# Optimization experiments

Measured on AMD Instinct MI355X. Metric: run time of the kernel, lower is better.

The kernel has to match this reference:

```python
import jax, jax.numpy as jnp
import numpy as np

NUM_CLASSES = 256


def setup_inputs() -> dict:
    key = jax.random.key(0)
    k1, k2 = jax.random.split(key)
    B = 524288
    logits = jax.random.normal(k1, (B, NUM_CLASSES), dtype=jnp.float32)
    targets = jax.random.randint(k2, (B,), 0, NUM_CLASSES, dtype=jnp.int64)
    return {"logits": logits, "targets": targets}


def reference(logits, targets):
    # cumulative logits along class dim: (B, C)
    cum = jnp.cumsum(logits, axis=1)
    C = logits.shape[1]
    # only thresholds k in [0, C-2] contribute (original loops range(C-1))
    ks = jnp.arange(C - 1)  # (C-1,)
    cum = cum[:, : C - 1]  # (B, C-1)
    # if k < target: loss += -logsigmoid(-cum[k]); else: loss += -logsigmoid(cum[k])
    sign = jnp.where(ks[None, :] < targets[:, None], -1.0, 1.0)  # (B, C-1)
    per_elem = -jax.nn.log_sigmoid(sign * cum)
    per_sample = jnp.sum(per_elem, axis=1)  # (B,)
    return jnp.mean(per_sample)
```

## Files before the change

kernel.cpp:

```cpp
#include <hip/hip_runtime.h>
#include <hip/hip_bf16.h>


#define WAVE 64
#define BLOCK 256
#define WPB (BLOCK / WAVE)
#define ROWS 8
#define NCLASS 256

__device__ __forceinline__ float wave_incl_scan(float s) {
    int t;
    t = __builtin_amdgcn_update_dpp(0, __float_as_int(s), 0x111, 0xf, 0xf, true); s += __int_as_float(t);
    t = __builtin_amdgcn_update_dpp(0, __float_as_int(s), 0x112, 0xf, 0xf, true); s += __int_as_float(t);
    t = __builtin_amdgcn_update_dpp(0, __float_as_int(s), 0x114, 0xf, 0xf, true); s += __int_as_float(t);
    t = __builtin_amdgcn_update_dpp(0, __float_as_int(s), 0x118, 0xf, 0xf, true); s += __int_as_float(t);
    t = __builtin_amdgcn_update_dpp(0, __float_as_int(s), 0x142, 0xa, 0xf, true); s += __int_as_float(t);
    t = __builtin_amdgcn_update_dpp(0, __float_as_int(s), 0x143, 0xc, 0xf, true); s += __int_as_float(t);
    return s;
}

template <bool EXACT>
__global__ __launch_bounds__(BLOCK) void ordloss_main(
        const float* __restrict__ logits,
        const int*   __restrict__ targets,
        double*      __restrict__ partials,
        int B) {
    const int lane = threadIdx.x & (WAVE - 1);
    const int wib  = threadIdx.x >> 6;
    const long long rowBase = ((long long)blockIdx.x * WPB + wib) * ROWS;
    const float lm = (lane == WAVE - 1) ? 0.0f : 1.0f;
    const int k0 = lane << 2;
    const float LOG2E = 1.4426950408889634f;

    const float4* p = reinterpret_cast<const float4*>(logits) + rowBase * (NCLASS / 4) + lane;

    float4 v[ROWS];
    int    tg[ROWS];
    #pragma unroll
    for (int i = 0; i < ROWS; ++i) {
        if (EXACT || rowBase + i < B) {
            v[i]  = p[i * (NCLASS / 4)];
            tg[i] = targets[rowBase + i];
        } else {
            v[i] = make_float4(0.f, 0.f, 0.f, 0.f);
            tg[i] = 0;
        }
    }

    float acc_lin = 0.0f, acc_abs = 0.0f, acc_log = 0.0f;
    #pragma unroll
    for (int i = 0; i < ROWS; ++i) {
        if (!EXACT && rowBase + i >= B) break;
        const int t = tg[i];

        const float l0 = v[i].x;
        const float l1 = l0 + v[i].y;
        const float l2 = l1 + v[i].z;
        const float l3 = l2 + v[i].w;

        const float incl = wave_incl_scan(l3);
        const float excl = incl - l3;

        const float c0 = excl + l0;
        const float c1 = excl + l1;
        const float c2 = excl + l2;
        const float c3 = excl + l3;

        const float a0 = fabsf(c0), a1 = fabsf(c1), a2 = fabsf(c2), a3 = fabsf(c3);

        const float u0 = __builtin_amdgcn_exp2f(-a0 * LOG2E);
        const float u1 = __builtin_amdgcn_exp2f(-a1 * LOG2E);
        const float u2 = __builtin_amdgcn_exp2f(-a2 * LOG2E);
        const float u3 = __builtin_amdgcn_exp2f(-a3 * LOG2E) * lm;

        float pr = 1.0f + u0;
        pr = __builtin_fmaf(pr, u1, pr);
        pr = __builtin_fmaf(pr, u2, pr);
        pr = __builtin_fmaf(pr, u3, pr);
        acc_log += __logf(pr);

        acc_abs += a0 + a1 + a2 + a3 * lm;

        const float sum_c = c0 + c1 + c2 + c3 * lm;
        float pre = 0.0f;
        pre += (k0 + 0 < t) ? c0 : 0.0f;
        pre += (k0 + 1 < t) ? c1 : 0.0f;
        pre += (k0 + 2 < t) ? c2 : 0.0f;
        pre += (k0 + 3 < t) ? c3 : 0.0f;
        acc_lin += 2.0f * pre - sum_c;
    }

    double d = 0.5 * ((double)acc_lin + (double)acc_abs) + (double)acc_log;
    #pragma unroll
    for (int off = 32; off > 0; off >>= 1)
        d += __shfl_down(d, off, WAVE);

    __shared__ double sd[WPB];
    if (lane == 0) sd[wib] = d;
    __syncthreads();
    if (threadIdx.x == 0) {
        double s = 0.0;
        #pragma unroll
        for (int w = 0; w < WPB; ++w) s += sd[w];
        partials[blockIdx.x] = s;
    }
}

__global__ __launch_bounds__(512) void ordloss_reduce(
        const double* __restrict__ partials, int n,
        float* __restrict__ out, double invB) {
    __shared__ double smem[512];
    double s = 0.0;
    for (int i = threadIdx.x; i < n; i += 512) s += partials[i];
    smem[threadIdx.x] = s;
    __syncthreads();
    for (int st = 256; st > 0; st >>= 1) {
        if (threadIdx.x < st) smem[threadIdx.x] += smem[threadIdx.x + st];
        __syncthreads();
    }
    if (threadIdx.x == 0) out[0] = (float)(smem[0] * invB);
}

extern "C" void kernel_launch(void* const* d_in, const int* in_sizes, int n_in,
                              void* d_out, int out_size, void* d_ws, size_t ws_size,
                              hipStream_t stream) {
    const float* logits   = (const float*)d_in[0];
    const int*   targets  = (const int*)d_in[1];
    float*       out      = (float*)d_out;
    double*      partials = (double*)d_ws;

    const int B = in_sizes[1];
    const int rows_per_block = WPB * ROWS;
    const int NB = (B + rows_per_block - 1) / rows_per_block;

    if (B % rows_per_block == 0)
        ordloss_main<true><<<NB, BLOCK, 0, stream>>>(logits, targets, partials, B);
    else
        ordloss_main<false><<<NB, BLOCK, 0, stream>>>(logits, targets, partials, B);

    ordloss_reduce<<<1, 512, 0, stream>>>(partials, NB, out, 1.0 / (double)B);
}
```

Before: 681.6 us.

## Use persistent grid-stride waves with double-buffered row batches and nontemporal loads

Replaces the one-shot grid, where each wave loaded 8 rows, with a fixed grid of 2048 blocks. Each wave now strides over batches of 4 rows and ping-pongs between two register buffers, so the next batch is loaded while the current one is computed. Logit loads become nontemporal to avoid cache pollution on a single streaming pass. This aims to hide memory latency and cut block launch overhead on a bandwidth-bound 512 MB read. The risks are higher register pressure and a possibly worse memory-level parallelism tradeoff.

```diff
diff --git a/kernel.cpp b/kernel.cpp
--- a/kernel.cpp
+++ b/kernel.cpp
@@ -1,12 +1,14 @@
 #include <hip/hip_runtime.h>
-#include <hip/hip_bf16.h>
 
 
 #define WAVE 64
 #define BLOCK 256
 #define WPB (BLOCK / WAVE)
-#define ROWS 8
+#define ROWS 4
 #define NCLASS 256
+#define NBLOCKS 2048
+
+typedef float v4f __attribute__((ext_vector_type(4)));
 
 __device__ __forceinline__ float wave_incl_scan(float s) {
     int t;
@@ -19,44 +21,38 @@
     return s;
 }
 
+struct Buf {
+    v4f v[ROWS];
+    int tg[ROWS];
+};
+
 template <bool EXACT>
-__global__ __launch_bounds__(BLOCK) void ordloss_main(
-        const float* __restrict__ logits,
-        const int*   __restrict__ targets,
-        double*      __restrict__ partials,
-        int B) {
-    const int lane = threadIdx.x & (WAVE - 1);
-    const int wib  = threadIdx.x >> 6;
-    const long long rowBase = ((long long)blockIdx.x * WPB + wib) * ROWS;
-    const float lm = (lane == WAVE - 1) ? 0.0f : 1.0f;
-    const int k0 = lane << 2;
-    const float LOG2E = 1.4426950408889634f;
-
-    const float4* p = reinterpret_cast<const float4*>(logits) + rowBase * (NCLASS / 4) + lane;
-
-    float4 v[ROWS];
-    int    tg[ROWS];
+__device__ __forceinline__ void load_batch(Buf& bf, const v4f* __restrict__ base,
+                                           const int* __restrict__ targets,
+                                           long long row0, int B) {
     #pragma unroll
     for (int i = 0; i < ROWS; ++i) {
-        if (EXACT || rowBase + i < B) {
-            v[i]  = p[i * (NCLASS / 4)];
-            tg[i] = targets[rowBase + i];
-        } else {
-            v[i] = make_float4(0.f, 0.f, 0.f, 0.f);
-            tg[i] = 0;
+        if (EXACT || row0 + i < B) {
+            bf.v[i]  = __builtin_nontemporal_load(base + (row0 + i) * (NCLASS / 4));
+            bf.tg[i] = targets[row0 + i];
         }
     }
+}
 
+template <bool EXACT>
+__device__ __forceinline__ void compute_batch(const Buf& bf, long long row0, int B,
+                                              int k0, float lm, double& dtot) {
+    const float LOG2E = 1.4426950408889634f;
     float acc_lin = 0.0f, acc_abs = 0.0f, acc_log = 0.0f;
     #pragma unroll
     for (int i = 0; i < ROWS; ++i) {
-        if (!EXACT && rowBase + i >= B) break;
-        const int t = tg[i];
+        if (!EXACT && row0 + i >= B) break;
+        const int t = bf.tg[i];
 
-        const float l0 = v[i].x;
-        const float l1 = l0 + v[i].y;
-        const float l2 = l1 + v[i].z;
-        const float l3 = l2 + v[i].w;
+        const float l0 = bf.v[i].x;
+        const float l1 = l0 + bf.v[i].y;
+        const float l2 = l1 + bf.v[i].z;
+        const float l3 = l2 + bf.v[i].w;
 
         const float incl = wave_incl_scan(l3);
         const float excl = incl - l3;
@@ -89,14 +85,59 @@
         pre += (k0 + 3 < t) ? c3 : 0.0f;
         acc_lin += 2.0f * pre - sum_c;
     }
+    dtot += 0.5 * ((double)acc_lin + (double)acc_abs) + (double)acc_log;
+}
 
-    double d = 0.5 * ((double)acc_lin + (double)acc_abs) + (double)acc_log;
+template <bool EXACT>
+__global__ __launch_bounds__(BLOCK) void ordloss_main(
+        const float* __restrict__ logits,
+        const int*   __restrict__ targets,
+        double*      __restrict__ partials,
+        int B) {
+    const int lane   = threadIdx.x & (WAVE - 1);
+    const int wib    = threadIdx.x >> 6;
+    const int waveId = blockIdx.x * WPB + wib;
+    const int nWaves = gridDim.x * WPB;
+    const float lm = (lane == WAVE - 1) ? 0.0f : 1.0f;
+    const int k0 = lane << 2;
+
+    const v4f* base = reinterpret_cast<const v4f*>(logits) + lane;
+    const long long nBatch = ((long long)B + ROWS - 1) / ROWS;
+
+    double dtot = 0.0;
+
+    long long bcur = waveId;
+    if (bcur < nBatch) {
+        Buf A, Bb;
+        load_batch<EXACT>(A, base, targets, bcur * ROWS, B);
+        for (;;) {
+            long long bnxt = bcur + nWaves;
+            if (bnxt < nBatch) {
+                load_batch<EXACT>(Bb, base, targets, bnxt * ROWS, B);
+                compute_batch<EXACT>(A, bcur * ROWS, B, k0, lm, dtot);
+                bcur = bnxt;
+                bnxt = bcur + nWaves;
+                if (bnxt < nBatch) {
+                    load_batch<EXACT>(A, base, targets, bnxt * ROWS, B);
+                    compute_batch<EXACT>(Bb, bcur * ROWS, B, k0, lm, dtot);
+                    bcur = bnxt;
+                } else {
+                    compute_batch<EXACT>(Bb, bcur * ROWS, B, k0, lm, dtot);
+                    break;
+                }
+            } else {
+                compute_batch<EXACT>(A, bcur * ROWS, B, k0, lm, dtot);
+                break;
+            }
+        }
+    }
+
     #pragma unroll
     for (int off = 32; off > 0; off >>= 1)
-        d += __shfl_down(d, off, WAVE);
+        dtot += __shfl_down(dtot, off, WAVE);
 
     __shared__ double sd[WPB];
-    if (lane == 0) sd[wib] = d;
+    if (lane == 0) sd[wib] = dtot;
     __syncthreads();
     if (threadIdx.x == 0) {
         double s = 0.0;
@@ -130,10 +171,11 @@
     double*      partials = (double*)d_ws;
 
     const int B = in_sizes[1];
-    const int rows_per_block = WPB * ROWS;
-    const int NB = (B + rows_per_block - 1) / rows_per_block;
+    const long long rows_per_block = (long long)WPB * ROWS;
+    long long nb_needed = ((long long)B + rows_per_block - 1) / rows_per_block;
+    const int NB = (int)(nb_needed < NBLOCKS ? nb_needed : NBLOCKS);
 
-    if (B % rows_per_block == 0)
+    if (B % ROWS == 0)
         ordloss_main<true><<<NB, BLOCK, 0, stream>>>(logits, targets, partials, B);
     else
         ordloss_main<false><<<NB, BLOCK, 0, stream>>>(logits, targets, partials, B);
```

Result: faster. 645.8 us (-5.2%).
